# Kernel tuning notes

Measured on AMD Instinct MI355X. Metric: run time of the kernel, lower is better.

Reference implementation:

```python
import jax, jax.numpy as jnp
import numpy as np

POOL = 2  # maxout pool size


def setup_inputs() -> dict:
    key = jax.random.key(0)
    ks = jax.random.split(key, 20)
    V, WV, ENC, DEC, ATT = 32000, 512, 512, 512, 512
    T, B, S, L = 32, 64, 256, 1
    IN = WV + ENC  # input_feed: emb concat context
    sc = 0.02
    emb_table = jax.random.normal(ks[0], (V, WV), jnp.float32) * sc
    emb_table = emb_table.at[0].set(0.0)  # padding_idx = PAD = 0
    inp = {
        'input_ids': jax.random.randint(ks[1], (T, B), 0, V),
        'hidden': jax.random.normal(ks[2], (L, B, DEC), jnp.float32),
        'context': jax.random.normal(ks[3], (S, B, ENC), jnp.float32),
        'src_pad_mask': jnp.zeros((B, S), jnp.float32),
        'init_att': jax.random.normal(ks[4], (B, ENC), jnp.float32),
        'emb_table': emb_table,
        'W_ih': jax.random.normal(ks[5], (3 * DEC, IN), jnp.float32) * sc,
        'W_hh': jax.random.normal(ks[6], (3 * DEC, DEC), jnp.float32) * sc,
        'b_ih': jnp.zeros((3 * DEC,), jnp.float32),
        'b_hh': jnp.zeros((3 * DEC,), jnp.float32),
        'W_pre': jax.random.normal(ks[7], (ATT, ENC), jnp.float32) * sc,
        'b_pre': jnp.zeros((ATT,), jnp.float32),
        'W_q': jax.random.normal(ks[8], (ATT, DEC), jnp.float32) * sc,
        'v_att': jax.random.normal(ks[9], (ATT,), jnp.float32) * sc,
        'W_copy': jax.random.normal(ks[10], (1, ENC + DEC), jnp.float32) * sc,
        'b_copy': jnp.zeros((1,), jnp.float32),
        'W_read': jax.random.normal(ks[11], (DEC, ENC + DEC + WV), jnp.float32) * sc,
        'b_read': jnp.zeros((DEC,), jnp.float32),
    }
    return inp


def reference(input_ids, hidden, context, src_pad_mask, init_att, emb_table,
              W_ih, W_hh, b_ih, b_hh, W_pre, b_pre, W_q, v_att,
              W_copy, b_copy, W_read, b_read):
    T, B = input_ids.shape
    dec = hidden.shape[-1]
    ctx_t = jnp.transpose(context, (1, 0, 2))            # [B, S, enc]
    # ConcatAttention precompute (done once, reused each step)
    precompute = jnp.einsum('bse,ae->bsa', ctx_t, W_pre) + b_pre  # [B, S, att]
    emb = emb_table[input_ids]                           # [T, B, wv]

    def gru_cell(x, h):
        gx = x @ W_ih.T + b_ih
        gh = h @ W_hh.T + b_hh
        xr, xz, xn = jnp.split(gx, 3, axis=-1)
        hr, hz, hn = jnp.split(gh, 3, axis=-1)
        r = jax.nn.sigmoid(xr + hr)
        z = jax.nn.sigmoid(xz + hz)
        n = jnp.tanh(xn + r * hn)
        return (1.0 - z) * n + z * h

    def step(carry, emb_t):
        h, cur_ctx = carry                               # h: [1,B,dec]
        x = jnp.concatenate([emb_t, cur_ctx], axis=1)    # input_feed
        h_new = gru_cell(x, h[0])
        out = h_new                                      # single layer output
        # concat attention
        target = out @ W_q.T                             # [B, att]
        tmp = jnp.tanh(precompute + target[:, None, :])  # [B, S, att]
        energy = jnp.einsum('bsa,a->bs', tmp, v_att)
        energy = energy * (1.0 - src_pad_mask) + src_pad_mask * (-1e6)
        score = jax.nn.softmax(energy, axis=-1)          # [B, S]
        new_ctx = jnp.einsum('bs,bse->be', score, ctx_t)
        # copy gate
        copy_p = jax.nn.sigmoid(
            jnp.concatenate([out, new_ctx], axis=1) @ W_copy.T + b_copy)
        # readout + maxout (dropout is identity at eval)
        readout = jnp.concatenate([emb_t, out, new_ctx], axis=1) @ W_read.T + b_read
        mo = readout.reshape(B, dec // POOL, POOL).max(axis=-1)
        return (h_new[None], new_ctx), (mo, score, copy_p)

    (hid, cur_ctx), (g_out, c_out, copy_out) = jax.lax.scan(
        step, (hidden, init_att), emb)
    return g_out, c_out, copy_out, hid, c_out[-1], cur_ctx
```

## Files before the change

### kernel.cpp

```cpp
#include <hip/hip_runtime.h>
#include <hip/hip_bf16.h>


typedef unsigned int uint;
typedef unsigned short ushort;
typedef __attribute__((ext_vector_type(8))) short s8v;
typedef __attribute__((ext_vector_type(4))) float f4v;

#define DD 512

__device__ __forceinline__ float sigmf(float x) { return 1.0f / (1.0f + __expf(-x)); }
__device__ __forceinline__ float tanh_fast(float x) {
    float e = __expf(2.0f * x);
    return 1.0f - 2.0f / (e + 1.0f);
}
__device__ __forceinline__ ushort f2bf(float f) {
    uint b = __float_as_uint(f);
    return (ushort)((b + 0x7FFFu + ((b >> 16) & 1u)) >> 16);
}
__device__ __forceinline__ uint pk2(float a, float b) {
    return (uint)f2bf(a) | ((uint)f2bf(b) << 16);
}
__device__ __forceinline__ float bfl(uint u) { return __uint_as_float(u << 16); }
__device__ __forceinline__ float bfh(uint u) { return __uint_as_float(u & 0xFFFF0000u); }
__device__ __forceinline__ f4v MFMA(s8v a, s8v b, f4v c) {
    return __builtin_amdgcn_mfma_f32_16x16x32_bf16(a, b, c, 0, 0, 0);
}

__device__ __forceinline__ void flag_bar(uint* arr, uint* rel, int member,
                                         int nmem, uint tag) {
    __syncthreads();
    const int tid = threadIdx.x;
    if (tid == 0) {
        asm volatile("s_waitcnt vmcnt(0) lgkmcnt(0)" ::: "memory");
        __hip_atomic_store(arr + member, tag, __ATOMIC_RELAXED,
                           __HIP_MEMORY_SCOPE_AGENT);
    }
    if (member == 0) {
        if (tid > 0 && tid < nmem) {
            while (__hip_atomic_load(arr + tid, __ATOMIC_RELAXED,
                                     __HIP_MEMORY_SCOPE_AGENT) < tag) {}
        }
        if (tid == 0)
            __hip_atomic_store(rel, tag, __ATOMIC_RELAXED,
                               __HIP_MEMORY_SCOPE_AGENT);
    } else {
        if (tid == 0) {
            while (__hip_atomic_load(rel, __ATOMIC_RELAXED,
                                     __HIP_MEMORY_SCOPE_AGENT) < tag) {}
        }
    }
    __syncthreads();
}

template <int MODE, int MT>
__device__ __forceinline__ void mgemm_body(
    const float* __restrict__ A0, const float* __restrict__ A1,
    const float* __restrict__ A2, const int* __restrict__ ids,
    const float* __restrict__ Bm, const float* __restrict__ bias,
    void* __restrict__ Cout, int ldb, int K, int bx, int by,
    ushort* Ab, ushort* Bb, int* rid)
{
    const int tid = threadIdx.x;
    const int m0 = bx * (MT * 16), n0 = by * 64;
    if (MODE != 0 && tid < MT * 16) rid[tid] = ids[m0 + tid];
    const int lane = tid & 63;
    const int w = tid >> 6;
    const int sc = tid & 3;
    f4v acc[MT];
#pragma unroll
    for (int mt = 0; mt < MT; ++mt) acc[mt] = (f4v){0.f, 0.f, 0.f, 0.f};

    for (int k0 = 0; k0 < K; k0 += 32) {
        __syncthreads();
#pragma unroll
        for (int p = 0; p < MT / 4; ++p) {
            int row = p * 64 + (tid >> 2);
            const float* ap;
            int m = m0 + row;
            if (MODE == 0) {
                ap = A0 + (size_t)(m & 255) * 32768 + (size_t)(m >> 8) * 512 + k0 + sc * 8;
            } else if (MODE == 1) {
                ap = A0 + (size_t)rid[row] * 512 + k0 + sc * 8;
            } else {
                if (k0 < 512)       ap = A0 + (size_t)rid[row] * 512 + k0 + sc * 8;
                else if (k0 < 1024) ap = A1 + (size_t)m * 512 + (k0 - 512) + sc * 8;
                else                ap = A2 + (size_t)m * 512 + (k0 - 1024) + sc * 8;
            }
            float4 v0 = *(const float4*)ap;
            float4 v1 = *(const float4*)(ap + 4);
            uint4 pa;
            pa.x = pk2(v0.x, v0.y); pa.y = pk2(v0.z, v0.w);
            pa.z = pk2(v1.x, v1.y); pa.w = pk2(v1.z, v1.w);
            *(uint4*)&Ab[row * 32 + ((sc ^ (row & 3)) << 3)] = pa;
        }
        {
            int row = tid >> 2;
            const float* bp = Bm + (size_t)(n0 + row) * ldb + k0 + sc * 8;
            float4 w0 = *(const float4*)bp;
            float4 w1 = *(const float4*)(bp + 4);
            uint4 pb;
            pb.x = pk2(w0.x, w0.y); pb.y = pk2(w0.z, w0.w);
            pb.z = pk2(w1.x, w1.y); pb.w = pk2(w1.z, w1.w);
            *(uint4*)&Bb[row * 32 + ((sc ^ (row & 3)) << 3)] = pb;
        }
        __syncthreads();
        int rr = lane & 15, kc = lane >> 4;
        s8v bf = *(const s8v*)&Bb[(w * 16 + rr) * 32 + ((kc ^ (rr & 3)) << 3)];
#pragma unroll
        for (int mt = 0; mt < MT; ++mt) {
            s8v af = *(const s8v*)&Ab[(mt * 16 + rr) * 32 + ((kc ^ (rr & 3)) << 3)];
            acc[mt] = MFMA(af, bf, acc[mt]);
        }
    }
    float bv = bias[n0 + w * 16 + (lane & 15)];
#pragma unroll
    for (int mt = 0; mt < MT; ++mt) {
#pragma unroll
        for (int r2 = 0; r2 < 4; ++r2) {
            int m = m0 + mt * 16 + (lane >> 4) * 4 + r2;
            int n = n0 + w * 16 + (lane & 15);
            float v = acc[mt][r2] + bv;
            if (MODE == 0) {
                ((ushort*)Cout)[(size_t)m * 512 + n] = f2bf(v);
            } else if (MODE == 1) {
                ((float*)Cout)[(size_t)m * 1536 + n] = v;
            } else {
                float vm = fmaxf(v, __shfl_xor(v, 1));
                if (!(lane & 1)) ((float*)Cout)[(size_t)m * 256 + (n >> 1)] = vm;
            }
        }
    }
}

__global__ __launch_bounds__(256) void k_prep(
    const float* __restrict__ context, const float* __restrict__ emb_t,
    const int* __restrict__ ids,
    const float* __restrict__ W_ih, const float* __restrict__ W_hh,
    const float* __restrict__ W_q, const float* __restrict__ W_pre,
    const float* __restrict__ b_pre, const float* __restrict__ b_ih,
    ushort* __restrict__ preb, float* __restrict__ gxe,
    uint* __restrict__ Wpk, uint* __restrict__ WqT, uint* __restrict__ cnt)
{
    __shared__ __align__(16) ushort Ab[8 * 16 * 32];
    __shared__ __align__(16) ushort Bb[64 * 32];
    __shared__ int rid[128];
    const int bid = blockIdx.x;
    if (bid < 1024) {
        mgemm_body<0, 8>(context, nullptr, nullptr, nullptr, W_pre, b_pre,
                         (void*)preb, 512, 512, bid & 127, bid >> 7, Ab, Bb, rid);
    } else if (bid < 1792) {
        int b2 = bid - 1024;
        mgemm_body<1, 4>(emb_t, nullptr, nullptr, ids, W_ih, b_ih,
                         (void*)gxe, 1024, 512, b2 & 31, b2 >> 5, Ab, Bb, rid);
    } else if (bid < 5376) {
        int id = (bid - 1792) * 256 + threadIdx.x;
        if (id < 786432) {
            int l4 = id & 255;
            int chunk = id >> 8;
            int g = chunk % 3;
            int t2 = chunk / 3;
            int ks = t2 & 15;
            int mat = (t2 >> 4) & 1;
            int u = t2 >> 5;
            int lane = l4 >> 2, e2 = l4 & 3;
            int n = g * 512 + u * 16 + (lane & 15);
            int k = ks * 32 + ((lane >> 4) << 3) + e2 * 2;
            float w0, w1;
            if (mat == 0) {
                w0 = W_ih[(size_t)n * 1024 + 512 + k];
                w1 = W_ih[(size_t)n * 1024 + 512 + k + 1];
            } else {
                w0 = W_hh[(size_t)n * 512 + k];
                w1 = W_hh[(size_t)n * 512 + k + 1];
            }
            Wpk[id] = pk2(w0, w1);
        } else {
            int rid2 = id - 786432;
            int kp = rid2 >> 9, a = rid2 & 511;
            WqT[rid2] = pk2(W_q[(size_t)a * 512 + 2 * kp],
                            W_q[(size_t)a * 512 + 2 * kp + 1]);
        }
    } else {
        int t4 = threadIdx.x * 16;
#pragma unroll
        for (int i = 0; i < 16; ++i) cnt[t4 + i] = 0;
    }
}

__global__ __launch_bounds__(512, 1) void k_steps(
    const float* __restrict__ gxe, const float* __restrict__ hidden,
    const float* __restrict__ init_att, const float* __restrict__ context,
    const float* __restrict__ mask, const float* __restrict__ v_att,
    const float* __restrict__ b_hh, const ushort* __restrict__ preb,
    const uint* __restrict__ Wpk, const uint* __restrict__ WqT,
    float* __restrict__ h_hist, float* __restrict__ ctx_hist,
    float* __restrict__ pe_buf, uint* __restrict__ cnt,
    float* __restrict__ cout)
{
    __shared__ __align__(16) ushort preT[256 * 128];
    __shared__ __align__(16) ushort ctxT[256 * 128];
    __shared__ __align__(16) float scr[6144];
    __shared__ float smask[256];
    __shared__ float svatt[128];

    const int tid = threadIdx.x;
    const int blk = blockIdx.x;
    const int q = blk >> 6;
    const int b = blk & 63;
    const int r = b & 7;
    const int u = ((b >> 3) << 2) | q;
    const int lane = tid & 63;
    const int wid = __builtin_amdgcn_readfirstlane(tid >> 6);

    uint* garr = cnt + r * 64;
    uint* grel = cnt + 512 + r * 16;
    uint* carr = cnt + 1024 + b * 8;
    uint* crel = cnt + 2048 + b * 16;

#pragma unroll
    for (int cc = 0; cc < 8; ++cc) {
        int cid = tid * 8 + cc;
        int s = cid >> 4, ch = cid & 15;
        int sw = (s ^ (s >> 3)) & 7;
        uint4 pv = *(const uint4*)(preb + ((size_t)(b * 256 + s)) * 512 + q * 128 + ch * 8);
        *(uint4*)&preT[s * 128 + ((ch ^ sw) << 3)] = pv;
        const float* cp = context + ((size_t)s * 64 + b) * 512 + q * 128 + ch * 8;
        float4 c0 = *(const float4*)cp;
        float4 c1 = *(const float4*)(cp + 4);
        uint4 cv;
        cv.x = pk2(c0.x, c0.y); cv.y = pk2(c0.z, c0.w);
        cv.z = pk2(c1.x, c1.y); cv.w = pk2(c1.z, c1.w);
        *(uint4*)&ctxT[s * 128 + ch * 8] = cv;
    }
    if (tid < 256) smask[tid] = mask[b * 256 + tid];
    else if (tid < 384) svatt[tid - 256] = v_att[q * 128 + (tid - 256)];

    const int mat_w = wid >> 2, kw = wid & 3;
    s8v wr0[4], wr1[4], wr2[4];
#pragma unroll
    for (int s = 0; s < 4; ++s) {
        int ks = kw * 4 + s;
        const uint* wb = Wpk + ((((u * 2 + mat_w) * 16 + ks) * 3) << 8) + (lane << 2);
        wr0[s] = *(const s8v*)(wb);
        wr1[s] = *(const s8v*)(wb + 256);
        wr2[s] = *(const s8v*)(wb + 512);
    }
    const int a_p2 = tid & 127, dq_p2 = tid >> 7;
    uint wqreg[64];
#pragma unroll
    for (int i = 0; i < 64; ++i)
        wqreg[i] = WqT[(size_t)(dq_p2 * 64 + i) * 512 + q * 128 + a_p2];

    const int bloc = tid >> 4, jj = tid & 15;
    int bb_c = 0, d_c = 0, eidx = 0;
    float bh0 = 0.f, bh1 = 0.f, bh2 = 0.f;
    if (tid < 128) {
        bb_c = r + bloc * 8;
        d_c = u * 16 + jj;
        eidx = ((jj + ((bloc >> 2) << 4)) << 2) + (bloc & 3);
        bh0 = b_hh[d_c]; bh1 = b_hh[512 + d_c]; bh2 = b_hh[1024 + d_c];
    }

    float gx0 = 0.f, gx1 = 0.f, gx2 = 0.f, hpv = 0.f;
    if (tid < 128) {
        const float* gp = gxe + (size_t)bb_c * 1536 + d_c;
        gx0 = gp[0]; gx1 = gp[512]; gx2 = gp[1024];
        hpv = hidden[(size_t)bb_c * 512 + d_c];
    }
    {
        int c = tid & 63, row = tid >> 6;
        int bb = r + row * 8;
        const float* sp0 = init_att + (size_t)bb * 512 + c * 8;
        float4 a0 = *(const float4*)sp0, a1 = *(const float4*)(sp0 + 4);
        uint4 p0;
        p0.x = pk2(a0.x, a0.y); p0.y = pk2(a0.z, a0.w);
        p0.z = pk2(a1.x, a1.y); p0.w = pk2(a1.z, a1.w);
        *(uint4*)((char*)scr + row * 1024 + ((c ^ row) << 4)) = p0;
        const float* sp1 = hidden + (size_t)bb * 512 + c * 8;
        float4 b0 = *(const float4*)sp1, b1 = *(const float4*)(sp1 + 4);
        uint4 p1;
        p1.x = pk2(b0.x, b0.y); p1.y = pk2(b0.z, b0.w);
        p1.z = pk2(b1.x, b1.y); p1.w = pk2(b1.z, b1.w);
        *(uint4*)((char*)scr + 8192 + row * 1024 + ((c ^ row) << 4)) = p1;
    }
    __syncthreads();

    for (int t = 0; t < 32; ++t) {
        f4v ac0 = (f4v){0.f, 0.f, 0.f, 0.f};
        f4v ac1 = ac0, ac2 = ac0;
        {
            const char* xbase = (const char*)scr + mat_w * 8192 + (lane & 15) * 1024;
            int rsw = (lane & 15) & 7;
#pragma unroll
            for (int s = 0; s < 4; ++s) {
                int ch = kw * 16 + s * 4 + (lane >> 4);
                s8v af = *(const s8v*)(xbase + ((ch ^ rsw) << 4));
                ac0 = MFMA(af, wr0[s], ac0);
                ac1 = MFMA(af, wr1[s], ac1);
                ac2 = MFMA(af, wr2[s], ac2);
            }
        }
        __syncthreads();
        {
            f4v* rb = (f4v*)scr;
            rb[((mat_w * 3 + 0) * 4 + kw) * 64 + lane] = ac0;
            rb[((mat_w * 3 + 1) * 4 + kw) * 64 + lane] = ac1;
            rb[((mat_w * 3 + 2) * 4 + kw) * 64 + lane] = ac2;
        }
        __syncthreads();
        if (tid < 128) {
            float AX[3], AH[3];
#pragma unroll
            for (int g = 0; g < 3; ++g) {
                float sx = 0.f, sh = 0.f;
#pragma unroll
                for (int kw2 = 0; kw2 < 4; ++kw2) {
                    sx += scr[((0 + g) * 4 + kw2) * 256 + eidx];
                    sh += scr[((3 + g) * 4 + kw2) * 256 + eidx];
                }
                AX[g] = sx;
                AH[g] = sh;
            }
            AX[0] += gx0; AX[1] += gx1; AX[2] += gx2;
            AH[0] += bh0; AH[1] += bh1; AH[2] += bh2;
            float rr = sigmf(AX[0] + AH[0]);
            float zz = sigmf(AX[1] + AH[1]);
            float nn = tanh_fast(AX[2] + rr * AH[2]);
            h_hist[(size_t)t * 32768 + (size_t)bb_c * 512 + d_c] =
                (1.0f - zz) * nn + zz * hpv;
        }
        flag_bar(garr, grel, u, 32, (uint)(t * 4 + 1));

        scr[tid] = h_hist[(size_t)t * 32768 + (size_t)b * 512 + tid];
        __syncthreads();
        {
            float acc = 0.f;
#pragma unroll
            for (int i = 0; i < 64; ++i) {
                uint w = wqreg[i];
                acc = fmaf(bfl(w), scr[(dq_p2 * 64 + i) * 2 + 0],
                           fmaf(bfh(w), scr[(dq_p2 * 64 + i) * 2 + 1], acc));
            }
            scr[512 + tid] = acc;
        }
        __syncthreads();
        if (tid < 128)
            scr[1024 + tid] = scr[512 + tid] + scr[640 + tid] +
                              scr[768 + tid] + scr[896 + tid];
        __syncthreads();

        {
            int s = tid & 255, hf = tid >> 8;
            int sw = (s ^ (s >> 3)) & 7;
            float acc = 0.f;
#pragma unroll
            for (int c8 = 0; c8 < 8; ++c8) {
                int ch = hf * 8 + c8;
                uint4 pv = *(const uint4*)&preT[s * 128 + ((ch ^ sw) << 3)];
                int ab = ch * 8;
                acc += svatt[ab + 0] * tanh_fast(bfl(pv.x) + scr[1024 + ab + 0]);
                acc += svatt[ab + 1] * tanh_fast(bfh(pv.x) + scr[1024 + ab + 1]);
                acc += svatt[ab + 2] * tanh_fast(bfl(pv.y) + scr[1024 + ab + 2]);
                acc += svatt[ab + 3] * tanh_fast(bfh(pv.y) + scr[1024 + ab + 3]);
                acc += svatt[ab + 4] * tanh_fast(bfl(pv.z) + scr[1024 + ab + 4]);
                acc += svatt[ab + 5] * tanh_fast(bfh(pv.z) + scr[1024 + ab + 5]);
                acc += svatt[ab + 6] * tanh_fast(bfl(pv.w) + scr[1024 + ab + 6]);
                acc += svatt[ab + 7] * tanh_fast(bfh(pv.w) + scr[1024 + ab + 7]);
            }
            scr[1280 + tid] = acc;
        }
        __syncthreads();
        if (tid < 256)
            pe_buf[((size_t)t * 64 + b) * 1024 + q * 256 + tid] =
                scr[1280 + tid] + scr[1536 + tid];
        flag_bar(carr, crel, q, 4, (uint)(t * 4 + 2));

        {
            int s2 = tid & 255;
            const float* peb = pe_buf + ((size_t)t * 64 + b) * 1024;
            float e = peb[s2] + peb[256 + s2] + peb[512 + s2] + peb[768 + s2];
            float mk = smask[s2];
            e = e * (1.0f - mk) + mk * (-1e6f);
            float mx = e;
#pragma unroll
            for (int off = 1; off < 64; off <<= 1) mx = fmaxf(mx, __shfl_xor(mx, off));
            if (lane == 0) scr[3072 + wid] = mx;
            __syncthreads();
            mx = scr[3072];
#pragma unroll
            for (int w2 = 1; w2 < 8; ++w2) mx = fmaxf(mx, scr[3072 + w2]);
            float ex = __expf(e - mx);
            float sm = ex;
#pragma unroll
            for (int off = 1; off < 64; off <<= 1) sm += __shfl_xor(sm, off);
            if (lane == 0) scr[3080 + wid] = sm;
            __syncthreads();
            sm = scr[3080] + scr[3081] + scr[3082] + scr[3083];
            float sc = ex / sm;
            scr[1792 + s2] = sc;
            if (q == 0 && tid < 256) cout[((size_t)t * 64 + b) * 256 + tid] = sc;
        }
        __syncthreads();
        {
            int e2 = tid & 63, sq = tid >> 6;
            float acc0 = 0.f, acc1 = 0.f;
#pragma unroll 8
            for (int i = 0; i < 32; ++i) {
                int ss = sq * 32 + i;
                uint cv = *(const uint*)&ctxT[ss * 128 + e2 * 2];
                float sc = scr[1792 + ss];
                acc0 = fmaf(sc, bfl(cv), acc0);
                acc1 = fmaf(sc, bfh(cv), acc1);
            }
            scr[2048 + sq * 128 + e2 * 2 + 0] = acc0;
            scr[2048 + sq * 128 + e2 * 2 + 1] = acc1;
        }
        __syncthreads();
        if (tid < 128) {
            float val = 0.f;
#pragma unroll
            for (int s8 = 0; s8 < 8; ++s8) val += scr[2048 + s8 * 128 + tid];
            ctx_hist[(size_t)t * 32768 + (size_t)b * 512 + q * 128 + tid] = val;
        }

        __syncthreads();
        if (tid == 0) {
            asm volatile("s_waitcnt vmcnt(0) lgkmcnt(0)" ::: "memory");
            __hip_atomic_store(garr + u, (uint)(t * 4 + 3), __ATOMIC_RELAXED,
                               __HIP_MEMORY_SCOPE_AGENT);
        }
        if (t < 31) {
            if (tid < 128) {
                const float* gp = gxe + ((size_t)(t + 1) * 64 + bb_c) * 1536 + d_c;
                gx0 = gp[0]; gx1 = gp[512]; gx2 = gp[1024];
                hpv = h_hist[(size_t)t * 32768 + (size_t)bb_c * 512 + d_c];
            }
            int c = tid & 63, row = tid >> 6;
            int bb = r + row * 8;
            const float* sp = h_hist + (size_t)t * 32768 + (size_t)bb * 512 + c * 8;
            float4 v0 = *(const float4*)sp, v1 = *(const float4*)(sp + 4);
            uint4 p1;
            p1.x = pk2(v0.x, v0.y); p1.y = pk2(v0.z, v0.w);
            p1.z = pk2(v1.x, v1.y); p1.w = pk2(v1.z, v1.w);
            *(uint4*)((char*)scr + 8192 + row * 1024 + ((c ^ row) << 4)) = p1;
        }
        if (u == 0) {
            if (tid > 0 && tid < 32) {
                while (__hip_atomic_load(garr + tid, __ATOMIC_RELAXED,
                                         __HIP_MEMORY_SCOPE_AGENT) < (uint)(t * 4 + 3)) {}
            }
            if (tid == 0)
                __hip_atomic_store(grel, (uint)(t * 4 + 3), __ATOMIC_RELAXED,
                                   __HIP_MEMORY_SCOPE_AGENT);
        } else {
            if (tid == 0) {
                while (__hip_atomic_load(grel, __ATOMIC_RELAXED,
                                         __HIP_MEMORY_SCOPE_AGENT) < (uint)(t * 4 + 3)) {}
            }
        }
        __syncthreads();
        if (t < 31) {
            int c = tid & 63, row = tid >> 6;
            int bb = r + row * 8;
            const float* sp = ctx_hist + (size_t)t * 32768 + (size_t)bb * 512 + c * 8;
            float4 v0 = *(const float4*)sp, v1 = *(const float4*)(sp + 4);
            uint4 p0;
            p0.x = pk2(v0.x, v0.y); p0.y = pk2(v0.z, v0.w);
            p0.z = pk2(v1.x, v1.y); p0.w = pk2(v1.z, v1.w);
            *(uint4*)((char*)scr + row * 1024 + ((c ^ row) << 4)) = p0;
        }
        __syncthreads();
    }
}

__global__ __launch_bounds__(256) void k_post(
    const float* __restrict__ emb_t, const int* __restrict__ ids,
    const float* __restrict__ h_hist, const float* __restrict__ ctx_hist,
    const float* __restrict__ W_read, const float* __restrict__ b_read,
    const float* __restrict__ W_copy, const float* __restrict__ b_copy,
    float* __restrict__ out)
{
    __shared__ __align__(16) ushort Ab[4 * 16 * 32];
    __shared__ __align__(16) ushort Bb[64 * 32];
    __shared__ int rid[64];
    const int bid = blockIdx.x;
    const int tid = threadIdx.x;
    if (bid < 256) {
        mgemm_body<2, 4>(emb_t, h_hist, ctx_hist, ids, W_read, b_read,
                         (void*)out, 1536, 1536, bid & 31, bid >> 5, Ab, Bb, rid);
    } else if (bid < 768) {
        const int lane = tid & 63;
        const int tb = (bid - 256) * 4 + (tid >> 6);
        const float* hp = h_hist + (size_t)tb * DD;
        const float* cp = ctx_hist + (size_t)tb * DD;
        float acc = 0.f;
#pragma unroll
        for (int jj = 0; jj < 8; ++jj) {
            int k = lane + 64 * jj;
            acc = fmaf(hp[k], W_copy[k], acc);
            acc = fmaf(cp[k], W_copy[512 + k], acc);
        }
#pragma unroll
        for (int off = 1; off < 64; off <<= 1) acc += __shfl_xor(acc, off);
        if (lane == 0) out[1048576 + tb] = sigmf(acc + b_copy[0]);
    } else {
        int idx = (bid - 768) * 256 + tid;
        if (idx < 32768) {
            out[1050624 + idx] = h_hist[31 * 32768 + idx];
        } else if (idx < 49152) {
            int i2 = idx - 32768;
            out[1083392 + i2] = out[524288 + 507904 + i2];
        } else {
            int i2 = idx - 49152;
            out[1099776 + i2] = ctx_hist[31 * 32768 + i2];
        }
    }
}

extern "C" void kernel_launch(void* const* d_in, const int* in_sizes, int n_in,
                              void* d_out, int out_size, void* d_ws, size_t ws_size,
                              hipStream_t stream)
{
    (void)in_sizes; (void)n_in; (void)out_size; (void)ws_size;
    const int*   ids      = (const int*)d_in[0];
    const float* hidden   = (const float*)d_in[1];
    const float* context  = (const float*)d_in[2];
    const float* mask     = (const float*)d_in[3];
    const float* init_att = (const float*)d_in[4];
    const float* emb_t    = (const float*)d_in[5];
    const float* W_ih     = (const float*)d_in[6];
    const float* W_hh     = (const float*)d_in[7];
    const float* b_ih     = (const float*)d_in[8];
    const float* b_hh     = (const float*)d_in[9];
    const float* W_pre    = (const float*)d_in[10];
    const float* b_pre    = (const float*)d_in[11];
    const float* W_q      = (const float*)d_in[12];
    const float* v_att    = (const float*)d_in[13];
    const float* W_copy   = (const float*)d_in[14];
    const float* b_copy   = (const float*)d_in[15];
    const float* W_read   = (const float*)d_in[16];
    const float* b_read   = (const float*)d_in[17];
    float* out = (float*)d_out;
    float* ws = (float*)d_ws;

    ushort* preb    = (ushort*)ws;
    float* gxe      = ws + 4194304;
    float* h_hist   = ws + 7340032;
    float* ctx_hist = ws + 8388608;
    float* pe_buf   = ws + 9437184;
    uint* Wpk       = (uint*)(ws + 11534336);
    uint* WqT       = (uint*)(ws + 12320768);
    uint* cnt       = (uint*)(ws + 12451840);
    float* cout     = out + 524288;

    k_prep<<<5377, 256, 0, stream>>>(context, emb_t, ids, W_ih, W_hh, W_q, W_pre,
                                     b_pre, b_ih, preb, gxe, Wpk, WqT, cnt);
    {
        void* args[] = {
            (void*)&gxe, (void*)&hidden, (void*)&init_att, (void*)&context,
            (void*)&mask, (void*)&v_att, (void*)&b_hh, (void*)&preb,
            (void*)&Wpk, (void*)&WqT,
            (void*)&h_hist, (void*)&ctx_hist, (void*)&pe_buf, (void*)&cnt,
            (void*)&cout
        };
        hipLaunchCooperativeKernel((void*)k_steps, dim3(256), dim3(512), args, 0,
                                   stream);
    }
    k_post<<<1088, 256, 0, stream>>>(emb_t, ids, h_hist, ctx_hist, W_read, b_read,
                                     W_copy, b_copy, out);
}
```

Baseline: 556.3 us.

## Split GRU recurrent MFMA by gate instead of K, drop cross-wave reduction

In the persistent step kernel, each of six waves now owns one (matrix, gate) pair and runs the full K=512 reduction with 16 register-held weight fragments. Previously eight waves each covered a quarter of K for all three gates, and their partial sums went through shared memory and were added back together. The new split drops that reduction and one __syncthreads per step, but it idles two waves during the MFMA phase and raises register pressure. Separately, the prep GEMM for W_pre uses 16-row tiles with half as many blocks, and the attention-score output write is spread across all four q-blocks.

Measured after the change: 608.4 us. 9.4% more time.

```diff
diff --git a/kernel.cpp b/kernel.cpp
--- a/kernel.cpp
+++ b/kernel.cpp
@@ -142,19 +142,19 @@
     ushort* __restrict__ preb, float* __restrict__ gxe,
     uint* __restrict__ Wpk, uint* __restrict__ WqT, uint* __restrict__ cnt)
 {
-    __shared__ __align__(16) ushort Ab[8 * 16 * 32];
+    __shared__ __align__(16) ushort Ab[16 * 16 * 32];
     __shared__ __align__(16) ushort Bb[64 * 32];
-    __shared__ int rid[128];
+    __shared__ int rid[256];
     const int bid = blockIdx.x;
-    if (bid < 1024) {
-        mgemm_body<0, 8>(context, nullptr, nullptr, nullptr, W_pre, b_pre,
-                         (void*)preb, 512, 512, bid & 127, bid >> 7, Ab, Bb, rid);
-    } else if (bid < 1792) {
-        int b2 = bid - 1024;
+    if (bid < 512) {
+        mgemm_body<0, 16>(context, nullptr, nullptr, nullptr, W_pre, b_pre,
+                          (void*)preb, 512, 512, bid & 63, bid >> 6, Ab, Bb, rid);
+    } else if (bid < 1280) {
+        int b2 = bid - 512;
         mgemm_body<1, 4>(emb_t, nullptr, nullptr, ids, W_ih, b_ih,
                          (void*)gxe, 1024, 512, b2 & 31, b2 >> 5, Ab, Bb, rid);
-    } else if (bid < 5376) {
-        int id = (bid - 1792) * 256 + threadIdx.x;
+    } else if (bid < 4864) {
+        int id = (bid - 1280) * 256 + threadIdx.x;
         if (id < 786432) {
             int l4 = id & 255;
             int chunk = id >> 8;
@@ -236,15 +236,15 @@
     if (tid < 256) smask[tid] = mask[b * 256 + tid];
     else if (tid < 384) svatt[tid - 256] = v_att[q * 128 + (tid - 256)];
 
-    const int mat_w = wid >> 2, kw = wid & 3;
-    s8v wr0[4], wr1[4], wr2[4];
-#pragma unroll
-    for (int s = 0; s < 4; ++s) {
-        int ks = kw * 4 + s;
-        const uint* wb = Wpk + ((((u * 2 + mat_w) * 16 + ks) * 3) << 8) + (lane << 2);
-        wr0[s] = *(const s8v*)(wb);
-        wr1[s] = *(const s8v*)(wb + 256);
-        wr2[s] = *(const s8v*)(wb + 512);
+    const int mat_w = wid & 1;
+    const int g_w = wid >> 1;
+    s8v wr[16];
+    if (g_w < 3) {
+#pragma unroll
+        for (int s = 0; s < 16; ++s) {
+            const uint* wb = Wpk + ((((u * 2 + mat_w) * 16 + s) * 3 + g_w) << 8) + (lane << 2);
+            wr[s] = *(const s8v*)wb;
+        }
     }
     const int a_p2 = tid & 127, dq_p2 = tid >> 7;
     uint wqreg[64];
@@ -287,40 +287,27 @@
     __syncthreads();
 
     for (int t = 0; t < 32; ++t) {
-        f4v ac0 = (f4v){0.f, 0.f, 0.f, 0.f};
-        f4v ac1 = ac0, ac2 = ac0;
-        {
+        if (g_w < 3) {
+            f4v ac = (f4v){0.f, 0.f, 0.f, 0.f};
             const char* xbase = (const char*)scr + mat_w * 8192 + (lane & 15) * 1024;
             int rsw = (lane & 15) & 7;
 #pragma unroll
-            for (int s = 0; s < 4; ++s) {
-                int ch = kw * 16 + s * 4 + (lane >> 4);
+            for (int s = 0; s < 16; ++s) {
+                int ch = s * 4 + (lane >> 4);
                 s8v af = *(const s8v*)(xbase + ((ch ^ rsw) << 4));
-                ac0 = MFMA(af, wr0[s], ac0);
-                ac1 = MFMA(af, wr1[s], ac1);
-                ac2 = MFMA(af, wr2[s], ac2);
-            }
-        }
-        __syncthreads();
-        {
-            f4v* rb = (f4v*)scr;
-            rb[((mat_w * 3 + 0) * 4 + kw) * 64 + lane] = ac0;
-            rb[((mat_w * 3 + 1) * 4 + kw) * 64 + lane] = ac1;
-            rb[((mat_w * 3 + 2) * 4 + kw) * 64 + lane] = ac2;
+                ac = MFMA(af, wr[s], ac);
+            }
+            f4v* rb = (f4v*)(scr + 4096);
+            rb[(mat_w * 3 + g_w) * 64 + lane] = ac;
         }
         __syncthreads();
         if (tid < 128) {
+            const float* rbf = scr + 4096;
             float AX[3], AH[3];
 #pragma unroll
             for (int g = 0; g < 3; ++g) {
-                float sx = 0.f, sh = 0.f;
-#pragma unroll
-                for (int kw2 = 0; kw2 < 4; ++kw2) {
-                    sx += scr[((0 + g) * 4 + kw2) * 256 + eidx];
-                    sh += scr[((3 + g) * 4 + kw2) * 256 + eidx];
-                }
-                AX[g] = sx;
-                AH[g] = sh;
+                AX[g] = rbf[(0 * 3 + g) * 256 + eidx];
+                AH[g] = rbf[(1 * 3 + g) * 256 + eidx];
             }
             AX[0] += gx0; AX[1] += gx1; AX[2] += gx2;
             AH[0] += bh0; AH[1] += bh1; AH[2] += bh2;
@@ -397,11 +384,11 @@
             if (lane == 0) scr[3080 + wid] = sm;
             __syncthreads();
             sm = scr[3080] + scr[3081] + scr[3082] + scr[3083];
-            float sc = ex / sm;
-            scr[1792 + s2] = sc;
-            if (q == 0 && tid < 256) cout[((size_t)t * 64 + b) * 256 + tid] = sc;
-        }
-        __syncthreads();
+            scr[1792 + s2] = ex / sm;
+        }
+        __syncthreads();
+        if (tid < 64)
+            cout[((size_t)t * 64 + b) * 256 + q * 64 + tid] = scr[1792 + q * 64 + tid];
         {
             int e2 = tid & 63, sq = tid >> 6;
             float acc0 = 0.f, acc1 = 0.f;
@@ -554,7 +541,7 @@
     uint* cnt       = (uint*)(ws + 12451840);
     float* cout     = out + 524288;
 
-    k_prep<<<5377, 256, 0, stream>>>(context, emb_t, ids, W_ih, W_hh, W_q, W_pre,
+    k_prep<<<4865, 256, 0, stream>>>(context, emb_t, ids, W_ih, W_hh, W_q, W_pre,
                                      b_pre, b_ih, preb, gxe, Wpk, WqT, cnt);
     {
         void* args[] = {
```
